# Performance work log

Measured on AMD Instinct MI355X. Metric: run time of the kernel, lower is better.

## Reference

```python
import jax, jax.numpy as jnp
import numpy as np

B, L, D, H = 4, 2048, 1024, 8
DH = D // H
NEG = float(-2**32 + 1)  # padding value used by the torch module


def setup_inputs() -> dict:
    key = jax.random.key(0)
    ks = jax.random.split(key, 7)
    queries = jax.random.normal(ks[0], (B, L, D), dtype=jnp.float32)
    keys = jax.random.normal(ks[1], (B, L, D), dtype=jnp.float32)
    sequence_length = jax.random.randint(ks[2], (B,), 1, L + 1, dtype=jnp.int32)
    scale = 0.02
    W_q = jax.random.normal(ks[3], (D, D), dtype=jnp.float32) * scale
    W_k = jax.random.normal(ks[4], (D, D), dtype=jnp.float32) * scale
    W_v = jax.random.normal(ks[5], (D, D), dtype=jnp.float32) * scale
    W_o = jax.random.normal(ks[6], (D, D), dtype=jnp.float32) * scale
    return {"queries": queries, "keys": keys, "sequence_length": sequence_length,
            "W_q": W_q, "W_k": W_k, "W_v": W_v, "W_o": W_o}


def reference(queries, keys, sequence_length, W_q, W_k, W_v, W_o):
    b, lq, d = queries.shape
    lk = keys.shape[1]
    # projections (nn.Linear, no bias): x @ W.T
    Q = (queries @ W_q.T).reshape(b, lq, H, DH).transpose(2, 0, 1, 3)  # (H,B,Lq,dh)
    K = (keys @ W_k.T).reshape(b, lk, H, DH).transpose(2, 0, 1, 3)
    V = (keys @ W_v.T).reshape(b, lk, H, DH).transpose(2, 0, 1, 3)
    scores = jnp.einsum('hbqd,hbkd->hbqk', Q, K) / jnp.sqrt(jnp.float32(DH))
    # additive key mask: positions >= sequence_length get large negative
    key_mask = jnp.arange(lk)[None, :] < sequence_length[:, None]      # (B,Lk)
    scores = jnp.where(key_mask[None, :, None, :], scores, NEG)
    attn = jax.nn.softmax(scores, axis=-1)
    # post-softmax multiplicative query mask
    q_mask = (jnp.arange(lq)[None, :] < sequence_length[:, None]).astype(attn.dtype)  # (B,Lq)
    attn = attn * q_mask[None, :, :, None]
    out = jnp.einsum('hbqk,hbkd->hbqd', attn, V)                       # (H,B,Lq,dh)
    # chunk-cat order: head h occupies columns h*dh:(h+1)*dh
    out = out.transpose(1, 2, 0, 3).reshape(b, lq, d)
    return out @ W_o.T  # dropout_rate=0 -> identity
```

## Files before the change

### kernel.cpp

```cpp
#include <hip/hip_runtime.h>
#include <math.h>

constexpr int Bsz = 4;
constexpr int Lsz = 2048;
constexpr int Dsz = 1024;
constexpr int Hn  = 8;
constexpr int Dh  = 128;
constexpr int GM  = Bsz * Lsz;
constexpr int GK  = Dsz;
constexpr int NT  = GK / 32;

typedef __attribute__((ext_vector_type(8))) short bf16x8;
typedef __attribute__((ext_vector_type(4))) float f32x4;

union FragU { unsigned int u[4]; bf16x8 f; };

__device__ __forceinline__ void gload16(const void* g, void* l) {
    __builtin_amdgcn_global_load_lds(
        (const __attribute__((address_space(1))) unsigned int*)g,
        (__attribute__((address_space(3))) unsigned int*)l, 16, 0, 0);
}

__device__ __forceinline__ void split2(float f0, float f1,
                                       unsigned int& hp, unsigned int& lp) {
    unsigned int u0 = __float_as_uint(f0), u1 = __float_as_uint(f1);
    hp = (u0 >> 16) | (u1 & 0xffff0000u);
    float l0 = f0 - __uint_as_float(u0 & 0xffff0000u);
    float l1 = f1 - __uint_as_float(u1 & 0xffff0000u);
    lp = (__float_as_uint(l0) >> 16) | (__float_as_uint(l1) & 0xffff0000u);
}

__device__ __forceinline__ void split4(float4 f, ushort4& h, ushort4& l2) {
    unsigned int ux = __float_as_uint(f.x), uy = __float_as_uint(f.y),
                 uz = __float_as_uint(f.z), uw = __float_as_uint(f.w);
    h.x = (unsigned short)(ux >> 16); h.y = (unsigned short)(uy >> 16);
    h.z = (unsigned short)(uz >> 16); h.w = (unsigned short)(uw >> 16);
    float lx = f.x - __uint_as_float(ux & 0xffff0000u);
    float ly = f.y - __uint_as_float(uy & 0xffff0000u);
    float lz = f.z - __uint_as_float(uz & 0xffff0000u);
    float lw = f.w - __uint_as_float(uw & 0xffff0000u);
    l2.x = (unsigned short)(__float_as_uint(lx) >> 16);
    l2.y = (unsigned short)(__float_as_uint(ly) >> 16);
    l2.z = (unsigned short)(__float_as_uint(lz) >> 16);
    l2.w = (unsigned short)(__float_as_uint(lw) >> 16);
}

struct WConv4 {
    const float4* w[4];
    ushort4* h[4];
    ushort4* l[4];
    float s[4];
};

__global__ __launch_bounds__(256) void conv_w4(WConv4 a) {
    int wi = blockIdx.x >> 10;
    int i = (blockIdx.x & 1023) * 256 + threadIdx.x;
    float4 f = a.w[wi][i];
    float s = a.s[wi];
    f.x *= s; f.y *= s; f.z *= s; f.w *= s;
    ushort4 h, l;
    split4(f, h, l);
    a.h[wi][i] = h; a.l[wi][i] = l;
}

__device__ __forceinline__ void compute_tile(const ushort* Ah, const ushort* Al,
                                             const ushort* Bh, const ushort* Bl,
                                             int wm, int wn, int l, int la,
                                             f32x4 acc[2][4]) {
    bf16x8 bh[4], bl4[4], ah[2], al[2];
#pragma unroll
    for (int fn = 0; fn < 4; ++fn) {
        int fng = wn * 4 + fn;
        bh[fn]  = *(const bf16x8*)&Bh[(fng * 64 + l) * 8];
        bl4[fn] = *(const bf16x8*)&Bl[(fng * 64 + l) * 8];
    }
#pragma unroll
    for (int fm = 0; fm < 2; ++fm) {
        int fmg = wm * 2 + fm;
        ah[fm] = *(const bf16x8*)&Ah[(fmg * 64 + la) * 8];
        al[fm] = *(const bf16x8*)&Al[(fmg * 64 + la) * 8];
    }
    __builtin_amdgcn_s_setprio(1);
#pragma unroll
    for (int fm = 0; fm < 2; ++fm)
#pragma unroll
        for (int fn = 0; fn < 4; ++fn) {
            acc[fm][fn] = __builtin_amdgcn_mfma_f32_16x16x32_bf16(
                ah[fm], bh[fn], acc[fm][fn], 0, 0, 0);
            acc[fm][fn] = __builtin_amdgcn_mfma_f32_16x16x32_bf16(
                ah[fm], bl4[fn], acc[fm][fn], 0, 0, 0);
            acc[fm][fn] = __builtin_amdgcn_mfma_f32_16x16x32_bf16(
                al[fm], bh[fn], acc[fm][fn], 0, 0, 0);
        }
    __builtin_amdgcn_s_setprio(0);
}

__device__ __forceinline__ void split_write(ushort* Ah, ushort* Al, int aw,
                                            float4 v0, float4 v1) {
    uint4 h4, l4;
    split2(v0.x, v0.y, h4.x, l4.x);
    split2(v0.z, v0.w, h4.y, l4.y);
    split2(v1.x, v1.y, h4.z, l4.z);
    split2(v1.z, v1.w, h4.w, l4.w);
    *(uint4*)&Ah[aw] = h4;
    *(uint4*)&Al[aw] = l4;
}

__global__ __launch_bounds__(512, 2) void gemm_qkv(
    const float* __restrict__ Aq, const float* __restrict__ Ak,
    const ushort* __restrict__ Wfh, const ushort* __restrict__ Wfl,
    ushort* __restrict__ Qhi, ushort* __restrict__ Qlo,
    ushort* __restrict__ Khi, ushort* __restrict__ Klo,
    ushort* __restrict__ Vthi, ushort* __restrict__ Vtlo,
    const int* __restrict__ slen)
{
    const int tid = threadIdx.x;
    const int bm = blockIdx.y << 7;
    const int bn = blockIdx.x << 7;
    const int grp = bn >> 10;

    const int nk = slen[bm >> 11];
    if ((bm & (Lsz - 1)) >= nk) return;

    __shared__ __align__(16) ushort lds[2][4][128 * 32];

    const float* A = (grp == 0) ? Aq : Ak;
    const int w  = tid >> 6;
    const int l  = tid & 63;
    const int wm = w >> 1;
    const int wn = w & 1;
    const int la = l ^ ((l >> 4) << 1);

    const int arow = tid >> 2;
    const int kg   = tid & 3;
    const float* ag = A + (size_t)(bm + arow) * GK + (kg << 3);
    const int aw = ((((arow >> 4) << 6) + (kg << 4) + ((arow & 15) ^ (kg << 1))) << 3);

    const int brow = ((tid >> 6) << 4) + (tid & 15);
    const int bkk  = ((tid >> 4) & 3) << 3;
    const ushort* bgh = Wfh + (size_t)(bn + brow) * GK + bkk;
    const ushort* bgl = Wfl + (size_t)(bn + brow) * GK + bkk;

    f32x4 acc[2][4];
#pragma unroll
    for (int i = 0; i < 2; ++i)
#pragma unroll
        for (int j = 0; j < 4; ++j) acc[i][j] = (f32x4)0.f;

    {
        float4 tC0 = *(const float4*)(ag);
        float4 tC1 = *(const float4*)(ag + 4);
        gload16(bgh, &lds[0][2][tid * 8]);
        gload16(bgl, &lds[0][3][tid * 8]);
        split_write(&lds[0][0][0], &lds[0][1][0], aw, tC0, tC1);
    }
    float4 rN0 = *(const float4*)(ag + 32);
    float4 rN1 = *(const float4*)(ag + 36);
    float4 rA0, rA1;
    __syncthreads();

    for (int t = 0; t < NT - 2; t += 2) {
        rA0 = *(const float4*)(ag + (t + 2) * 32);
        rA1 = *(const float4*)(ag + (t + 2) * 32 + 4);
        gload16(bgh + (t + 1) * 32, &lds[1][2][tid * 8]);
        gload16(bgl + (t + 1) * 32, &lds[1][3][tid * 8]);
        split_write(&lds[1][0][0], &lds[1][1][0], aw, rN0, rN1);
        compute_tile(&lds[0][0][0], &lds[0][1][0], &lds[0][2][0], &lds[0][3][0],
                     wm, wn, l, la, acc);
        __syncthreads();

        rN0 = *(const float4*)(ag + (t + 3) * 32);
        rN1 = *(const float4*)(ag + (t + 3) * 32 + 4);
        gload16(bgh + (t + 2) * 32, &lds[0][2][tid * 8]);
        gload16(bgl + (t + 2) * 32, &lds[0][3][tid * 8]);
        split_write(&lds[0][0][0], &lds[0][1][0], aw, rA0, rA1);
        compute_tile(&lds[1][0][0], &lds[1][1][0], &lds[1][2][0], &lds[1][3][0],
                     wm, wn, l, la, acc);
        __syncthreads();
    }

    gload16(bgh + (NT - 1) * 32, &lds[1][2][tid * 8]);
    gload16(bgl + (NT - 1) * 32, &lds[1][3][tid * 8]);
    split_write(&lds[1][0][0], &lds[1][1][0], aw, rN0, rN1);
    compute_tile(&lds[0][0][0], &lds[0][1][0], &lds[0][2][0], &lds[0][3][0],
                 wm, wn, l, la, acc);
    __syncthreads();

    compute_tile(&lds[1][0][0], &lds[1][1][0], &lds[1][2][0], &lds[1][3][0],
                 wm, wn, l, la, acc);

    const int rq = (l >> 4) << 2;
    const int cq = l & 15;
    ushort* OH = (grp == 0) ? Qhi : Khi;
    ushort* OL = (grp == 0) ? Qlo : Klo;
#pragma unroll
    for (int fm = 0; fm < 2; ++fm) {
        int r0 = bm + wm * 32 + fm * 16 + rq;
#pragma unroll
        for (int fn = 0; fn < 4; ++fn) {
            int cn = (bn & 1023) + wn * 64 + fn * 16 + cq;
            if (grp < 2) {
#pragma unroll
                for (int r = 0; r < 4; ++r) {
                    float f = acc[fm][fn][r];
                    unsigned int u = __float_as_uint(f);
                    float res = f - __uint_as_float(u & 0xffff0000u);
                    OH[(size_t)(r0 + r) * Dsz + cn] = (unsigned short)(u >> 16);
                    OL[(size_t)(r0 + r) * Dsz + cn] =
                        (unsigned short)(__float_as_uint(res) >> 16);
                }
            } else {
                ushort4 h4, l4;
                unsigned short* hp = (unsigned short*)&h4;
                unsigned short* lp = (unsigned short*)&l4;
#pragma unroll
                for (int r = 0; r < 4; ++r) {
                    float f = acc[fm][fn][r];
                    unsigned int u = __float_as_uint(f);
                    float res = f - __uint_as_float(u & 0xffff0000u);
                    hp[r] = (unsigned short)(u >> 16);
                    lp[r] = (unsigned short)(__float_as_uint(res) >> 16);
                }
                *(ushort4*)&Vthi[(size_t)cn * GM + r0] = h4;
                *(ushort4*)&Vtlo[(size_t)cn * GM + r0] = l4;
            }
        }
    }
}

__global__ __launch_bounds__(512, 2) void gemm_o(
    const ushort* __restrict__ Ahi, const ushort* __restrict__ Alo,
    const ushort* __restrict__ Bhi, const ushort* __restrict__ Blo,
    float* __restrict__ C, const int* __restrict__ slen)
{
    const int tid = threadIdx.x;
    const int bm = blockIdx.y << 7;
    const int bn = blockIdx.x << 7;

    const int nk = slen[bm >> 11];
    if ((bm & (Lsz - 1)) >= nk) {
        int row = tid >> 2;
        int cb  = (tid & 3) << 5;
        float4 z = make_float4(0.f, 0.f, 0.f, 0.f);
        float4* cp = (float4*)(C + (size_t)(bm + row) * Dsz + bn + cb);
#pragma unroll
        for (int i = 0; i < 8; ++i) cp[i] = z;
        return;
    }

    __shared__ __align__(16) ushort lds[2][4][128 * 32];

    const int w  = tid >> 6;
    const int l  = tid & 63;
    const int wm = w >> 1;
    const int wn = w & 1;

    const int srow = ((tid >> 6) << 4) + (tid & 15);
    const int skk  = ((tid >> 4) & 3) << 3;
    const ushort* agh = Ahi + (size_t)(bm + srow) * GK + skk;
    const ushort* agl = Alo + (size_t)(bm + srow) * GK + skk;
    const ushort* bgh = Bhi + (size_t)(bn + srow) * GK + skk;
    const ushort* bgl = Blo + (size_t)(bn + srow) * GK + skk;

    f32x4 acc[2][4];
#pragma unroll
    for (int i = 0; i < 2; ++i)
#pragma unroll
        for (int j = 0; j < 4; ++j) acc[i][j] = (f32x4)0.f;

    gload16(agh, &lds[0][0][tid * 8]);
    gload16(agl, &lds[0][1][tid * 8]);
    gload16(bgh, &lds[0][2][tid * 8]);
    gload16(bgl, &lds[0][3][tid * 8]);
    __syncthreads();

    for (int t = 0; t < NT - 1; ++t) {
        const int p = t & 1;
        const int q = p ^ 1;
        gload16(agh + (t + 1) * 32, &lds[q][0][tid * 8]);
        gload16(agl + (t + 1) * 32, &lds[q][1][tid * 8]);
        gload16(bgh + (t + 1) * 32, &lds[q][2][tid * 8]);
        gload16(bgl + (t + 1) * 32, &lds[q][3][tid * 8]);
        compute_tile(&lds[p][0][0], &lds[p][1][0], &lds[p][2][0], &lds[p][3][0],
                     wm, wn, l, l, acc);
        __syncthreads();
    }
    {
        const int p = (NT - 1) & 1;
        compute_tile(&lds[p][0][0], &lds[p][1][0], &lds[p][2][0], &lds[p][3][0],
                     wm, wn, l, l, acc);
    }

    const int rq = (l >> 4) << 2;
    const int cq = l & 15;
#pragma unroll
    for (int fm = 0; fm < 2; ++fm) {
        int r0 = bm + wm * 32 + fm * 16 + rq;
#pragma unroll
        for (int fn = 0; fn < 4; ++fn) {
            int c0 = bn + wn * 64 + fn * 16 + cq;
#pragma unroll
            for (int r = 0; r < 4; ++r)
                C[(size_t)(r0 + r) * Dsz + c0] = acc[fm][fn][r];
        }
    }
}

__global__ __launch_bounds__(256) void flash_mfma(
    const ushort* __restrict__ Qhi, const ushort* __restrict__ Qlo,
    const ushort* __restrict__ Khi, const ushort* __restrict__ Klo,
    const ushort* __restrict__ Vthi, const ushort* __restrict__ Vtlo,
    const int* __restrict__ slen,
    ushort* __restrict__ Ohi, ushort* __restrict__ Olo)
{
    __shared__ __align__(16) ushort Ks[32 * 256];
    __shared__ __align__(16) ushort Vs[128 * 64];
    __shared__ __align__(16) unsigned int Pb[4 * 16 * 36];

    const int tid = threadIdx.x;
    const int w = tid >> 6, l = tid & 63;
    const int lg = l >> 4, lc = l & 15;
    const int q0 = blockIdx.x << 6;
    const int h = blockIdx.y, b = blockIdx.z;
    const int nk = slen[b];

    if ((q0 & ~127) >= nk) return;

    if (q0 >= nk) {
#pragma unroll
        for (int rr = 0; rr < 4; ++rr) {
            int q = q0 + (w << 4) + (lg << 2) + rr;
            size_t base = (size_t)(b * Lsz + q) * Dsz + h * Dh + lc;
#pragma unroll
            for (int fd = 0; fd < 8; ++fd) {
                Ohi[base + fd * 16] = 0;
                Olo[base + fd * 16] = 0;
            }
        }
        return;
    }

    bf16x8 qh[4], ql[4];
    {
        size_t base = (size_t)(b * Lsz + q0 + (w << 4) + lc) * Dsz + h * Dh + lg * 8;
#pragma unroll
        for (int s = 0; s < 4; ++s) {
            qh[s] = *(const bf16x8*)&Qhi[base + s * 32];
            ql[s] = *(const bf16x8*)&Qlo[base + s * 32];
        }
    }

    const ushort* ksrc[4]; int klds[4];
    const ushort* vsrc[4]; int vlds[4];
#pragma unroll
    for (int i = 0; i < 4; ++i) {
        int s = i * 256 + tid;
        int j = s >> 5, p = s & 31;
        int lg4 = (p & 15) ^ (j & 15);
        const ushort* base = (p & 16) ? Klo : Khi;
        ksrc[i] = base + (size_t)(b * Lsz + j) * Dsz + h * Dh + lg4 * 8;
        klds[i] = s * 8;
    }
#pragma unroll
    for (int i = 0; i < 4; ++i) {
        int s = i * 256 + tid;
        int d = s >> 3, p = s & 7;
        int lgc = p ^ (d & 7);
        const ushort* base = (lgc & 4) ? Vtlo : Vthi;
        vsrc[i] = base + (size_t)(h * Dh + d) * (Bsz * Lsz) + b * Lsz + (lgc & 3) * 8;
        vlds[i] = s * 8;
    }

    f32x4 oacc[8];
#pragma unroll
    for (int fd = 0; fd < 8; ++fd) oacc[fd] = (f32x4)0.f;
    float lsum[4] = {0.f, 0.f, 0.f, 0.f};
    const int pbase = w * (16 * 36);

    for (int kb = 0; kb < nk; kb += 32) {
#pragma unroll
        for (int i = 0; i < 4; ++i) gload16(ksrc[i] + (size_t)kb * Dsz, &Ks[klds[i]]);
#pragma unroll
        for (int i = 0; i < 4; ++i) gload16(vsrc[i] + kb, &Vs[vlds[i]]);
        __syncthreads();

        f32x4 sa[2] = {(f32x4)0.f, (f32x4)0.f};
        __builtin_amdgcn_s_setprio(1);
#pragma unroll
        for (int fn = 0; fn < 2; ++fn) {
            int j = fn * 16 + lc;
            int ro = j * 256;
#pragma unroll
            for (int s = 0; s < 4; ++s) {
                int phys = (s * 4 + lg) ^ (j & 15);
                bf16x8 kh = *(const bf16x8*)&Ks[ro + phys * 8];
                bf16x8 kl = *(const bf16x8*)&Ks[ro + 128 + phys * 8];
                sa[fn] = __builtin_amdgcn_mfma_f32_16x16x32_bf16(qh[s], kh, sa[fn], 0, 0, 0);
                sa[fn] = __builtin_amdgcn_mfma_f32_16x16x32_bf16(qh[s], kl, sa[fn], 0, 0, 0);
                sa[fn] = __builtin_amdgcn_mfma_f32_16x16x32_bf16(ql[s], kh, sa[fn], 0, 0, 0);
            }
        }
        __builtin_amdgcn_s_setprio(0);

        if (kb + 32 > nk) {
#pragma unroll
            for (int fn = 0; fn < 2; ++fn) {
                bool oob = (kb + fn * 16 + lc) >= nk;
#pragma unroll
                for (int rr = 0; rr < 4; ++rr)
                    sa[fn][rr] = oob ? -1e30f : sa[fn][rr];
            }
        }

#pragma unroll
        for (int fn = 0; fn < 2; ++fn)
#pragma unroll
            for (int rr = 0; rr < 4; ++rr) {
                float p = __expf(sa[fn][rr]);
                lsum[rr] += p;
                unsigned int u = __float_as_uint(p);
                float res = p - __uint_as_float(u & 0xffff0000u);
                unsigned int lo16 = __float_as_uint(res) >> 16;
                Pb[pbase + (lg * 4 + rr) * 36 + fn * 16 + lc] =
                    (lo16 << 16) | (u >> 16);
            }

        const unsigned int* pr = &Pb[pbase + lc * 36 + lg * 8];
        uint4 a0 = *(const uint4*)pr;
        uint4 a1 = *(const uint4*)(pr + 4);
        FragU PH, PL;
        PH.u[0] = (a0.x & 0xffffu) | (a0.y << 16);
        PH.u[1] = (a0.z & 0xffffu) | (a0.w << 16);
        PH.u[2] = (a1.x & 0xffffu) | (a1.y << 16);
        PH.u[3] = (a1.z & 0xffffu) | (a1.w << 16);
        PL.u[0] = (a0.x >> 16) | (a0.y & 0xffff0000u);
        PL.u[1] = (a0.z >> 16) | (a0.w & 0xffff0000u);
        PL.u[2] = (a1.x >> 16) | (a1.y & 0xffff0000u);
        PL.u[3] = (a1.z >> 16) | (a1.w & 0xffff0000u);

        __builtin_amdgcn_s_setprio(1);
#pragma unroll
        for (int fd = 0; fd < 8; ++fd) {
            int d = fd * 16 + lc;
            int ro = d * 64;
            int ph = lg ^ (d & 7);
            int pl2 = (4 + lg) ^ (d & 7);
            bf16x8 vh = *(const bf16x8*)&Vs[ro + ph * 8];
            bf16x8 vl = *(const bf16x8*)&Vs[ro + pl2 * 8];
            oacc[fd] = __builtin_amdgcn_mfma_f32_16x16x32_bf16(PH.f, vh, oacc[fd], 0, 0, 0);
            oacc[fd] = __builtin_amdgcn_mfma_f32_16x16x32_bf16(PH.f, vl, oacc[fd], 0, 0, 0);
            oacc[fd] = __builtin_amdgcn_mfma_f32_16x16x32_bf16(PL.f, vh, oacc[fd], 0, 0, 0);
        }
        __builtin_amdgcn_s_setprio(0);
        __syncthreads();
    }

#pragma unroll
    for (int m = 1; m < 16; m <<= 1)
#pragma unroll
        for (int rr = 0; rr < 4; ++rr)
            lsum[rr] += __shfl_xor(lsum[rr], m, 64);

#pragma unroll
    for (int rr = 0; rr < 4; ++rr) {
        int q = q0 + (w << 4) + (lg << 2) + rr;
        bool valid = q < nk;
        float inv = valid ? (1.f / lsum[rr]) : 0.f;
        size_t base = (size_t)(b * Lsz + q) * Dsz + h * Dh + lc;
#pragma unroll
        for (int fd = 0; fd < 8; ++fd) {
            float val = valid ? oacc[fd][rr] * inv : 0.f;
            unsigned int u = __float_as_uint(val);
            float res = val - __uint_as_float(u & 0xffff0000u);
            Ohi[base + fd * 16] = (unsigned short)(u >> 16);
            Olo[base + fd * 16] = (unsigned short)(__float_as_uint(res) >> 16);
        }
    }
}

extern "C" void kernel_launch(void* const* d_in, const int* in_sizes, int n_in,
                              void* d_out, int out_size, void* d_ws, size_t ws_size,
                              hipStream_t stream) {
    (void)in_sizes; (void)n_in; (void)out_size; (void)ws_size;
    const float* queries = (const float*)d_in[0];
    const float* keys    = (const float*)d_in[1];
    const int*   slen    = (const int*)d_in[2];
    const float* Wq      = (const float*)d_in[3];
    const float* Wk      = (const float*)d_in[4];
    const float* Wv      = (const float*)d_in[5];
    const float* Wo      = (const float*)d_in[6];
    float* out = (float*)d_out;

    const size_t MD = (size_t)Bsz * Lsz * Dsz;
    const size_t WD = (size_t)Dsz * Dsz;
    ushort* Qhi  = (ushort*)d_ws;
    ushort* Qlo  = Qhi + MD;
    ushort* Khi  = Qlo + MD;
    ushort* Klo  = Khi + MD;
    ushort* Vthi = Klo + MD;
    ushort* Vtlo = Vthi + MD;
    ushort* Wfh  = Vtlo + MD;
    ushort* Wfl  = Wfh + 3 * WD;
    ushort* Woh  = Wfl + 3 * WD;
    ushort* Wol  = Woh + WD;

    const float scaleQ = 0.08838834764831845f;
    WConv4 wa;
    wa.w[0] = (const float4*)Wq; wa.h[0] = (ushort4*)Wfh;            wa.l[0] = (ushort4*)Wfl;            wa.s[0] = scaleQ;
    wa.w[1] = (const float4*)Wk; wa.h[1] = (ushort4*)(Wfh + WD);     wa.l[1] = (ushort4*)(Wfl + WD);     wa.s[1] = 1.f;
    wa.w[2] = (const float4*)Wv; wa.h[2] = (ushort4*)(Wfh + 2 * WD); wa.l[2] = (ushort4*)(Wfl + 2 * WD); wa.s[2] = 1.f;
    wa.w[3] = (const float4*)Wo; wa.h[3] = (ushort4*)Woh;            wa.l[3] = (ushort4*)Wol;            wa.s[3] = 1.f;
    conv_w4<<<4096, 256, 0, stream>>>(wa);

    gemm_qkv<<<dim3(24, 64), 512, 0, stream>>>(
        queries, keys, Wfh, Wfl, Qhi, Qlo, Khi, Klo, Vthi, Vtlo, slen);

    dim3 ga(Lsz / 64, Hn, Bsz);
    flash_mfma<<<ga, 256, 0, stream>>>(Qhi, Qlo, Khi, Klo, Vthi, Vtlo, slen,
                                       Qhi, Qlo );

    gemm_o<<<dim3(8, 64), 512, 0, stream>>>(Qhi, Qlo, Woh, Wol, out, slen);
}
```

Before: 385.5 us.

## Single-buffer QKV GEMM LDS and raise occupancy hint

```diff
diff --git a/kernel.cpp b/kernel.cpp
--- a/kernel.cpp
+++ b/kernel.cpp
@@ -106,7 +106,7 @@
     *(uint4*)&Al[aw] = l4;
 }
 
-__global__ __launch_bounds__(512, 2) void gemm_qkv(
+__global__ __launch_bounds__(512, 8) void gemm_qkv(
     const float* __restrict__ Aq, const float* __restrict__ Ak,
     const ushort* __restrict__ Wfh, const ushort* __restrict__ Wfl,
     ushort* __restrict__ Qhi, ushort* __restrict__ Qlo,
@@ -122,7 +122,7 @@
     const int nk = slen[bm >> 11];
     if ((bm & (Lsz - 1)) >= nk) return;
 
-    __shared__ __align__(16) ushort lds[2][4][128 * 32];
+    __shared__ __align__(16) ushort lds[4][128 * 32];
 
     const float* A = (grp == 0) ? Aq : Ak;
     const int w  = tid >> 6;
@@ -147,47 +147,22 @@
 #pragma unroll
         for (int j = 0; j < 4; ++j) acc[i][j] = (f32x4)0.f;
 
-    {
-        float4 tC0 = *(const float4*)(ag);
-        float4 tC1 = *(const float4*)(ag + 4);
-        gload16(bgh, &lds[0][2][tid * 8]);
-        gload16(bgl, &lds[0][3][tid * 8]);
-        split_write(&lds[0][0][0], &lds[0][1][0], aw, tC0, tC1);
-    }
-    float4 rN0 = *(const float4*)(ag + 32);
-    float4 rN1 = *(const float4*)(ag + 36);
-    float4 rA0, rA1;
-    __syncthreads();
-
-    for (int t = 0; t < NT - 2; t += 2) {
-        rA0 = *(const float4*)(ag + (t + 2) * 32);
-        rA1 = *(const float4*)(ag + (t + 2) * 32 + 4);
-        gload16(bgh + (t + 1) * 32, &lds[1][2][tid * 8]);
-        gload16(bgl + (t + 1) * 32, &lds[1][3][tid * 8]);
-        split_write(&lds[1][0][0], &lds[1][1][0], aw, rN0, rN1);
-        compute_tile(&lds[0][0][0], &lds[0][1][0], &lds[0][2][0], &lds[0][3][0],
+    float4 c0 = *(const float4*)(ag);
+    float4 c1 = *(const float4*)(ag + 4);
+
+    for (int t = 0; t < NT; ++t) {
+        gload16(bgh + t * 32, &lds[2][tid * 8]);
+        gload16(bgl + t * 32, &lds[3][tid * 8]);
+        split_write(&lds[0][0], &lds[1][0], aw, c0, c1);
+        __syncthreads();
+        if (t + 1 < NT) {
+            c0 = *(const float4*)(ag + (t + 1) * 32);
+            c1 = *(const float4*)(ag + (t + 1) * 32 + 4);
+        }
+        compute_tile(&lds[0][0], &lds[1][0], &lds[2][0], &lds[3][0],
                      wm, wn, l, la, acc);
         __syncthreads();
-
-        rN0 = *(const float4*)(ag + (t + 3) * 32);
-        rN1 = *(const float4*)(ag + (t + 3) * 32 + 4);
-        gload16(bgh + (t + 2) * 32, &lds[0][2][tid * 8]);
-        gload16(bgl + (t + 2) * 32, &lds[0][3][tid * 8]);
-        split_write(&lds[0][0][0], &lds[0][1][0], aw, rA0, rA1);
-        compute_tile(&lds[1][0][0], &lds[1][1][0], &lds[1][2][0], &lds[1][3][0],
-                     wm, wn, l, la, acc);
-        __syncthreads();
-    }
-
-    gload16(bgh + (NT - 1) * 32, &lds[1][2][tid * 8]);
-    gload16(bgl + (NT - 1) * 32, &lds[1][3][tid * 8]);
-    split_write(&lds[1][0][0], &lds[1][1][0], aw, rN0, rN1);
-    compute_tile(&lds[0][0][0], &lds[0][1][0], &lds[0][2][0], &lds[0][3][0],
-                 wm, wn, l, la, acc);
-    __syncthreads();
-
-    compute_tile(&lds[1][0][0], &lds[1][1][0], &lds[1][2][0], &lds[1][3][0],
-                 wm, wn, l, la, acc);
+    }
 
     const int rq = (l >> 4) << 2;
     const int cq = l & 15;
```

After: 1.348 ms. +249.6%, slower.
